# Kernel optimization log

Hardware: AMD Instinct MI355X
Metric: run time of the kernel (lower is better)

## Reference

```python
import math
import jax, jax.numpy as jnp
import numpy as np

B, L, D = 16, 2048, 64  # batch, seq len (m == n, self-attention), head dim
C = 30                   # ProbSparse sampling factor c


def setup_inputs() -> dict:
    key = jax.random.key(0)
    kq, kk, kv = jax.random.split(key, 3)
    Q = jax.random.normal(kq, (B, L, D), dtype=jnp.float32)
    K = jax.random.normal(kk, (B, L, D), dtype=jnp.float32)
    V = jax.random.normal(kv, (B, L, D), dtype=jnp.float32)
    return {"Q": Q, "K": K, "V": V, "seed": 0}


def reference(Q, K, V, seed):
    b, m, d = Q.shape
    n = K.shape[1]
    u = int(C * math.log(m))              # number of active queries
    U = min(int(m * math.log(n)), n)      # number of sampled keys (clamped to n)
    inv_sqrt_d = 1.0 / math.sqrt(d)

    rngs = jax.random.split(jax.random.key(seed), b)

    def _each_sample(Qb, Kb, Vb, r):
        # random sample of U key rows without replacement
        idx = jax.random.choice(r, n, shape=(U,), replace=False)
        Kbar = Kb[idx]                                # [U, d]
        Sbar = jnp.matmul(Qb, Kbar.T)                 # [m, U]
        M = jnp.max(Sbar, axis=1) - jnp.mean(Sbar, axis=1)  # sparsity measure [m]
        _, I = jax.lax.top_k(M, u)                    # active query indices [u]
        Qbar = Qb[I]                                  # [u, d]
        A = jax.nn.softmax(jnp.matmul(Qbar, Kb.T) * inv_sqrt_d, axis=-1)  # [u, n]
        S1 = jnp.matmul(A, Vb)                        # [u, d]
        # literal source: fill with mean(V, axis=1, keepdims=True) -> (n,1) broadcast (m==n)
        S = jnp.broadcast_to(jnp.mean(Vb, axis=1, keepdims=True), (m, d))
        return S.at[I].set(S1)

    return jax.vmap(_each_sample)(Q, K, V, rngs)
```

## Files before the change

kernel.cpp:

```cpp
#include <hip/hip_runtime.h>

#define NB 16
#define NN 2048
#define DH 64
#define NSEL 228
#define KS 8
#define CHUNK (NN / KS)
#define RS 4
#define EPSBAND 2.0e-3f

using s16x8 = __attribute__((ext_vector_type(8))) short;
using f32x16 = __attribute__((ext_vector_type(16))) float;

static __device__ __forceinline__ unsigned short f2bf(float x) {
  unsigned int u = __float_as_uint(x);
  u += 0x7fffu + ((u >> 16) & 1u);
  return (unsigned short)(u >> 16);
}
static __device__ __forceinline__ float bf2f(unsigned short h) {
  return __uint_as_float(((unsigned int)h) << 16);
}
static __device__ __forceinline__ unsigned int enc(float f) {
  unsigned int u = __float_as_uint(f);
  return (u & 0x80000000u) ? ~u : (u | 0x80000000u);
}
static __device__ __forceinline__ float dec(unsigned int k) {
  return (k & 0x80000000u) ? __uint_as_float(k & 0x7fffffffu)
                           : __uint_as_float(~k);
}

__global__ __launch_bounds__(256) void convk_kernel(const float* __restrict__ K,
                                                    unsigned short* __restrict__ Khi,
                                                    unsigned short* __restrict__ Klo) {
  const size_t e = ((size_t)blockIdx.x * 256 + threadIdx.x) * 8;
  float4 a = *(const float4*)(K + e);
  float4 b = *(const float4*)(K + e + 4);
  float v[8] = {a.x, a.y, a.z, a.w, b.x, b.y, b.z, b.w};
  union { unsigned short u[8]; s16x8 s; } H, L;
  #pragma unroll
  for (int j = 0; j < 8; ++j) {
    unsigned short h = f2bf(v[j]);
    H.u[j] = h;
    L.u[j] = f2bf(v[j] - bf2f(h));
  }
  *(s16x8*)(Khi + e) = H.s;
  *(s16x8*)(Klo + e) = L.s;
}

__global__ __launch_bounds__(256) void kcolsum_kernel(const float* __restrict__ K,
                                                      float* __restrict__ Kpart) {
  __shared__ float part[4][64];
  const int b = blockIdx.y, ch = blockIdx.x;
  const int d = threadIdx.x & 63, g = threadIdx.x >> 6;
  const float* Kb = K + ((size_t)b * NN + ch * 128) * DH;
  float s = 0.f;
  for (int r = g; r < 128; r += 4) s += Kb[r * DH + d];
  part[g][d] = s;
  __syncthreads();
  if (threadIdx.x < 64)
    Kpart[((size_t)b * 16 + ch) * 64 + threadIdx.x] =
        part[0][threadIdx.x] + part[1][threadIdx.x] +
        part[2][threadIdx.x] + part[3][threadIdx.x];
}

__global__ __launch_bounds__(256, 4) void rowstat_mfma(const float* __restrict__ Q,
                                                       const unsigned short* __restrict__ Khi,
                                                       const unsigned short* __restrict__ Klo,
                                                       float* __restrict__ Mmax) {
  __shared__ __align__(16) unsigned short KHs[128 * 64];
  __shared__ __align__(16) unsigned short KLs[128 * 64];
  const int b = blockIdx.y, cz = blockIdx.z;
  const int qbase = blockIdx.x * 128;
  const int tid = threadIdx.x;
  const int w = tid >> 6, lane = tid & 63;
  const int l31 = lane & 31, hi5 = lane >> 5;

  s16x8 qh[4], ql[4];
  {
    const float* qrow = Q + ((size_t)b * NN + qbase + w * 32 + l31) * DH;
    #pragma unroll
    for (int ks = 0; ks < 4; ++ks) {
      const int d0 = ks * 16 + hi5 * 8;
      float4 x = *(const float4*)(qrow + d0);
      float4 y = *(const float4*)(qrow + d0 + 4);
      float v[8] = {x.x, x.y, x.z, x.w, y.x, y.y, y.z, y.w};
      union { unsigned short u[8]; s16x8 s; } H, L;
      #pragma unroll
      for (int j = 0; j < 8; ++j) {
        unsigned short h = f2bf(v[j]);
        H.u[j] = h;
        L.u[j] = f2bf(v[j] - bf2f(h));
      }
      qh[ks] = H.s;
      ql[ks] = L.s;
    }
  }

  const size_t kbase = ((size_t)b * NN + cz * (NN / RS)) * DH;
  f32x16 vmax;
  #pragma unroll
  for (int i = 0; i < 16; ++i) vmax[i] = -3.0e38f;

  const int sr = tid >> 1;
  const int sh = tid & 1;

  for (int stage = 0; stage < NN / RS / 128; ++stage) {
    __syncthreads();
    {
      const size_t g = kbase + (size_t)(stage * 128 + sr) * DH + sh * 32;
      const unsigned short* gh = Khi + g;
      const unsigned short* gl = Klo + g;
      #pragma unroll
      for (int c = 0; c < 4; ++c) {
        s16x8 hv = *(const s16x8*)(gh + c * 8);
        s16x8 lv = *(const s16x8*)(gl + c * 8);
        const int chn = (sh * 4 + c) ^ (sr & 7);
        *(s16x8*)&KHs[(sr * 8 + chn) * 8] = hv;
        *(s16x8*)&KLs[(sr * 8 + chn) * 8] = lv;
      }
    }
    __syncthreads();

    #pragma unroll
    for (int ksub = 0; ksub < 4; ++ksub) {
      const int kr = ksub * 32 + l31;
      f32x16 acc;
      #pragma unroll
      for (int i = 0; i < 16; ++i) acc[i] = 0.f;
      #pragma unroll
      for (int ks = 0; ks < 4; ++ks) {
        const int chn = (ks * 2 + hi5) ^ (kr & 7);
        s16x8 ah = *(const s16x8*)&KHs[(kr * 8 + chn) * 8];
        s16x8 al = *(const s16x8*)&KLs[(kr * 8 + chn) * 8];
        acc = __builtin_amdgcn_mfma_f32_32x32x16_bf16(ah, qh[ks], acc, 0, 0, 0);
        acc = __builtin_amdgcn_mfma_f32_32x32x16_bf16(al, qh[ks], acc, 0, 0, 0);
        acc = __builtin_amdgcn_mfma_f32_32x32x16_bf16(ah, ql[ks], acc, 0, 0, 0);
      }
      #pragma unroll
      for (int i = 0; i < 16; ++i) vmax[i] = fmaxf(vmax[i], acc[i]);
    }
  }

  float m = vmax[0];
  #pragma unroll
  for (int i = 1; i < 16; ++i) m = fmaxf(m, vmax[i]);
  m = fmaxf(m, __shfl_xor(m, 32));
  if (lane < 32)
    Mmax[((size_t)cz * NB + b) * NN + qbase + w * 32 + lane] = m;
}

static __device__ unsigned int radix_thresh(const unsigned int* kreg, int lane,
                                            int wid, int* red) {
  unsigned int v = 0u;
  for (int bit = 31; bit >= 0; --bit) {
    const unsigned int cand = v | (1u << bit);
    int c = 0;
    #pragma unroll
    for (int f = 0; f < 8; ++f) c += (kreg[f] >= cand) ? 1 : 0;
    #pragma unroll
    for (int off = 1; off < 64; off <<= 1) c += __shfl_xor(c, off);
    if (lane == 0) red[wid] = c;
    __syncthreads();
    if (red[0] + red[1] + red[2] + red[3] >= NSEL) v = cand;
    __syncthreads();
  }
  return v;
}

__global__ __launch_bounds__(256) void select_kernel(const float* __restrict__ Q,
                                                     const float* __restrict__ K,
                                                     const float* __restrict__ Mmax,
                                                     const float* __restrict__ Kpart,
                                                     int* __restrict__ Isel) {
  __shared__ unsigned int keys[NN];
  __shared__ float meanv[NN];
  __shared__ int list_[NN];
  __shared__ float qsh[64];
  __shared__ float Ksl[64];
  __shared__ float fred[4];
  __shared__ int red[4];
  __shared__ int cntS;
  const int b = blockIdx.x;
  const int tid = threadIdx.x;
  const int lane = tid & 63, wid = tid >> 6;
  const int base = tid * 8;

  if (tid < 64) {
    float s = 0.f;
    for (int c = 0; c < 16; ++c) s += Kpart[((size_t)b * 16 + c) * 64 + tid];
    Ksl[tid] = s;
  }
  if (tid == 0) cntS = 0;
  __syncthreads();

  for (int f = 0; f < 8; ++f) {
    const int i = base + f;
    float mv = -3.0e38f;
    #pragma unroll
    for (int cz = 0; cz < RS; ++cz)
      mv = fmaxf(mv, Mmax[((size_t)cz * NB + b) * NN + i]);
    const float* qrow = Q + ((size_t)b * NN + i) * DH;
    float s = 0.f;
    #pragma unroll
    for (int d4 = 0; d4 < 16; ++d4) {
      float4 qv = *(const float4*)(qrow + d4 * 4);
      s = fmaf(qv.x, Ksl[d4 * 4 + 0], s);
      s = fmaf(qv.y, Ksl[d4 * 4 + 1], s);
      s = fmaf(qv.z, Ksl[d4 * 4 + 2], s);
      s = fmaf(qv.w, Ksl[d4 * 4 + 3], s);
    }
    const float mean = s * (1.0f / NN);
    meanv[i] = mean;
    keys[i] = enc(mv - mean);
  }
  __syncthreads();

  unsigned int kreg[8];
  #pragma unroll
  for (int f = 0; f < 8; ++f) kreg[f] = keys[base + f];

  const unsigned int v1 = radix_thresh(kreg, lane, wid, red);
  const float vf = dec(v1);

  #pragma unroll
  for (int f = 0; f < 8; ++f) {
    if (fabsf(dec(kreg[f]) - vf) <= EPSBAND) {
      int p = atomicAdd(&cntS, 1);
      list_[p] = base + f;
    }
  }
  __syncthreads();
  const int nband = cntS;
  for (int n = 0; n < nband; ++n) {
    const int row = list_[n];
    if (tid < 64) qsh[tid] = Q[((size_t)b * NN + row) * DH + tid];
    __syncthreads();
    float lmax = -3.0e38f;
    for (int j = tid; j < NN; j += 256) {
      const float* krow = K + ((size_t)b * NN + j) * DH;
      float s = 0.f;
      #pragma unroll
      for (int d4 = 0; d4 < 16; ++d4) {
        float4 kv = *(const float4*)(krow + d4 * 4);
        s = fmaf(kv.x, qsh[d4 * 4 + 0], s);
        s = fmaf(kv.y, qsh[d4 * 4 + 1], s);
        s = fmaf(kv.z, qsh[d4 * 4 + 2], s);
        s = fmaf(kv.w, qsh[d4 * 4 + 3], s);
      }
      lmax = fmaxf(lmax, s);
    }
    #pragma unroll
    for (int off = 1; off < 64; off <<= 1) lmax = fmaxf(lmax, __shfl_xor(lmax, off));
    if (lane == 0) fred[wid] = lmax;
    __syncthreads();
    if (tid == 0) {
      const float mx = fmaxf(fmaxf(fred[0], fred[1]), fmaxf(fred[2], fred[3]));
      keys[row] = enc(mx - meanv[row]);
    }
    __syncthreads();
  }
  #pragma unroll
  for (int f = 0; f < 8; ++f) kreg[f] = keys[base + f];

  const unsigned int v2 = radix_thresh(kreg, lane, wid, red);

  int flg[8];
  int cnt = 0;
  #pragma unroll
  for (int f = 0; f < 8; ++f) { flg[f] = (kreg[f] > v2) ? 1 : 0; cnt += flg[f]; }
  int scan = cnt;
  #pragma unroll
  for (int off = 1; off < 64; off <<= 1) {
    const int t = __shfl_up(scan, off);
    if (lane >= off) scan += t;
  }
  if (lane == 63) red[wid] = scan;
  __syncthreads();
  int wbase = 0;
  for (int ww = 0; ww < wid; ++ww) wbase += red[ww];
  const int cg = red[0] + red[1] + red[2] + red[3];
  int pos = wbase + scan - cnt;
  #pragma unroll
  for (int f = 0; f < 8; ++f)
    if (flg[f]) { Isel[b * NSEL + pos] = base + f; ++pos; }
  __syncthreads();

  const int need = NSEL - cg;
  cnt = 0;
  #pragma unroll
  for (int f = 0; f < 8; ++f) { flg[f] = (kreg[f] == v2) ? 1 : 0; cnt += flg[f]; }
  scan = cnt;
  #pragma unroll
  for (int off = 1; off < 64; off <<= 1) {
    const int t = __shfl_up(scan, off);
    if (lane >= off) scan += t;
  }
  if (lane == 63) red[wid] = scan;
  __syncthreads();
  wbase = 0;
  for (int ww = 0; ww < wid; ++ww) wbase += red[ww];
  pos = wbase + scan - cnt;
  #pragma unroll
  for (int f = 0; f < 8; ++f)
    if (flg[f]) {
      if (pos < need) Isel[b * NSEL + cg + pos] = base + f;
      ++pos;
    }
}

__global__ __launch_bounds__(256) void fill_kernel(const float* __restrict__ V,
                                                   float* __restrict__ out) {
  const size_t row = (size_t)blockIdx.x * 4 + (threadIdx.x >> 6);
  const int lane = threadIdx.x & 63;
  float x = V[row * DH + lane];
  #pragma unroll
  for (int off = 1; off < 64; off <<= 1) x += __shfl_xor(x, off);
  out[row * DH + lane] = x * (1.0f / DH);
}

__global__ __launch_bounds__(256) void attn_part_kernel(const float* __restrict__ Q,
                                                        const float* __restrict__ K,
                                                        const float* __restrict__ V,
                                                        const int* __restrict__ Isel,
                                                        float* __restrict__ Pm,
                                                        float* __restrict__ Pl,
                                                        float* __restrict__ Po) {
  __shared__ float Qt[64][32];
  __shared__ float Kt[64][64];
  __shared__ float Vs[64][64];
  __shared__ float Pt[64][36];
  const int b = blockIdx.z;
  const int kc = blockIdx.y;
  const int g = blockIdx.x;
  const int tid = threadIdx.x;
  const int wq = tid >> 5;
  const int kx = tid & 31;

  if (tid < 128) {
    const int rr = tid >> 2;
    const int dblk = (tid & 3) * 16;
    const int lq = g * 32 + rr;
    const int qidx = (lq < NSEL) ? Isel[b * NSEL + lq] : 0;
    const float* qs = Q + ((size_t)b * NN + qidx) * DH + dblk;
    #pragma unroll
    for (int f = 0; f < 4; ++f) {
      float4 v = *reinterpret_cast<const float4*>(qs + f * 4);
      Qt[dblk + f * 4 + 0][rr] = v.x;
      Qt[dblk + f * 4 + 1][rr] = v.y;
      Qt[dblk + f * 4 + 2][rr] = v.z;
      Qt[dblk + f * 4 + 3][rr] = v.w;
    }
  }

  const float* Kb = K + ((size_t)b * NN + kc * CHUNK) * DH;
  const float* Vb = V + ((size_t)b * NN + kc * CHUNK) * DH;

  float m[4], lp[4], o[4][2];
  #pragma unroll
  for (int a = 0; a < 4; ++a) {
    m[a] = -3.0e38f; lp[a] = 0.f; o[a][0] = 0.f; o[a][1] = 0.f;
  }

  for (int st = 0; st < CHUNK / 64; ++st) {
    __syncthreads();
    {
      const int rr = tid & 63;
      const int dblk = (tid >> 6) * 16;
      const float* ks = Kb + ((size_t)(st * 64 + rr)) * DH + dblk;
      #pragma unroll
      for (int f = 0; f < 4; ++f) {
        float4 v = *reinterpret_cast<const float4*>(ks + f * 4);
        Kt[dblk + f * 4 + 0][rr] = v.x;
        Kt[dblk + f * 4 + 1][rr] = v.y;
        Kt[dblk + f * 4 + 2][rr] = v.z;
        Kt[dblk + f * 4 + 3][rr] = v.w;
      }
      const float* vsrc = Vb + (size_t)st * 64 * DH;
      float* vdst = &Vs[0][0];
      #pragma unroll
      for (int it = 0; it < 4; ++it) {
        const int fo = (it * 256 + tid) * 4;
        *reinterpret_cast<float4*>(vdst + fo) =
            *reinterpret_cast<const float4*>(vsrc + fo);
      }
    }
    __syncthreads();

    float sc[4][2];
    #pragma unroll
    for (int a = 0; a < 4; ++a) { sc[a][0] = 0.f; sc[a][1] = 0.f; }
    #pragma unroll 4
    for (int d = 0; d < 64; ++d) {
      float qv[4];
      *reinterpret_cast<float4*>(qv) =
          *reinterpret_cast<const float4*>(&Qt[d][wq * 4]);
      const float2 kv = *reinterpret_cast<const float2*>(&Kt[d][kx * 2]);
      #pragma unroll
      for (int a = 0; a < 4; ++a) {
        sc[a][0] = fmaf(qv[a], kv.x, sc[a][0]);
        sc[a][1] = fmaf(qv[a], kv.y, sc[a][1]);
      }
    }
    #pragma unroll
    for (int a = 0; a < 4; ++a) { sc[a][0] *= 0.125f; sc[a][1] *= 0.125f; }

    float tm[4];
    #pragma unroll
    for (int a = 0; a < 4; ++a) tm[a] = fmaxf(sc[a][0], sc[a][1]);
    #pragma unroll
    for (int off = 1; off < 32; off <<= 1) {
      #pragma unroll
      for (int a = 0; a < 4; ++a) tm[a] = fmaxf(tm[a], __shfl_xor(tm[a], off));
    }

    float w0[4], w1[4];
    #pragma unroll
    for (int a = 0; a < 4; ++a) {
      const float mn = fmaxf(m[a], tm[a]);
      const float scale = __expf(m[a] - mn);
      m[a] = mn;
      lp[a] *= scale;
      o[a][0] *= scale;
      o[a][1] *= scale;
      w0[a] = __expf(sc[a][0] - mn);
      w1[a] = __expf(sc[a][1] - mn);
      lp[a] += w0[a] + w1[a];
    }
    *reinterpret_cast<float4*>(&Pt[kx * 2][wq * 4]) =
        make_float4(w0[0], w0[1], w0[2], w0[3]);
    *reinterpret_cast<float4*>(&Pt[kx * 2 + 1][wq * 4]) =
        make_float4(w1[0], w1[1], w1[2], w1[3]);
    __syncthreads();

    #pragma unroll 4
    for (int k = 0; k < 64; ++k) {
      float pv[4];
      *reinterpret_cast<float4*>(pv) =
          *reinterpret_cast<const float4*>(&Pt[k][wq * 4]);
      const float2 vv = *reinterpret_cast<const float2*>(&Vs[k][kx * 2]);
      #pragma unroll
      for (int a = 0; a < 4; ++a) {
        o[a][0] = fmaf(pv[a], vv.x, o[a][0]);
        o[a][1] = fmaf(pv[a], vv.y, o[a][1]);
      }
    }
  }

  #pragma unroll
  for (int off = 1; off < 32; off <<= 1) {
    #pragma unroll
    for (int a = 0; a < 4; ++a) lp[a] += __shfl_xor(lp[a], off);
  }

  #pragma unroll
  for (int a = 0; a < 4; ++a) {
    const int lq = g * 32 + wq * 4 + a;
    if (lq < NSEL) {
      const size_t row = ((size_t)b * NSEL + lq) * KS + kc;
      if (kx == 0) { Pm[row] = m[a]; Pl[row] = lp[a]; }
      *reinterpret_cast<float2*>(Po + row * 64 + kx * 2) =
          make_float2(o[a][0], o[a][1]);
    }
  }
}

__global__ __launch_bounds__(256) void combine_kernel(const int* __restrict__ Isel,
                                                      const float* __restrict__ Pm,
                                                      const float* __restrict__ Pl,
                                                      const float* __restrict__ Po,
                                                      float* __restrict__ out) {
  const int r = blockIdx.x * 4 + (threadIdx.x >> 6);
  if (r >= NB * NSEL) return;
  const int lane = threadIdx.x & 63;
  const int b = r / NSEL;
  const int qidx = Isel[r];
  const size_t base = (size_t)r * KS;

  float pm[KS];
  float gm = -3.0e38f;
  #pragma unroll
  for (int c = 0; c < KS; ++c) { pm[c] = Pm[base + c]; gm = fmaxf(gm, pm[c]); }
  float L = 0.f, od = 0.f;
  #pragma unroll
  for (int c = 0; c < KS; ++c) {
    const float e = __expf(pm[c] - gm);
    L += Pl[base + c] * e;
    od += Po[(base + c) * 64 + lane] * e;
  }
  out[((size_t)b * NN + qidx) * DH + lane] = od / L;
}

extern "C" void kernel_launch(void* const* d_in, const int* in_sizes, int n_in,
                              void* d_out, int out_size, void* d_ws, size_t ws_size,
                              hipStream_t stream) {
  const float* Q = (const float*)d_in[0];
  const float* K = (const float*)d_in[1];
  const float* V = (const float*)d_in[2];
  float* out = (float*)d_out;

  float* Mmax = (float*)d_ws;
  float* Kpart = Mmax + (size_t)RS * NB * NN;
  int* Isel = (int*)(Kpart + (size_t)NB * 16 * 64);
  float* Pm = (float*)(Isel + NB * NSEL);
  float* Pl = Pm + (size_t)NB * NSEL * KS;
  float* Po = Pl + (size_t)NB * NSEL * KS;
  unsigned short* Khi = (unsigned short*)(Po + (size_t)NB * NSEL * KS * 64);
  unsigned short* Klo = Khi + (size_t)NB * NN * DH;

  convk_kernel<<<dim3((NB * NN * DH) / (256 * 8)), 256, 0, stream>>>(K, Khi, Klo);
  kcolsum_kernel<<<dim3(16, NB), 256, 0, stream>>>(K, Kpart);
  rowstat_mfma<<<dim3(NN / 128, NB, RS), 256, 0, stream>>>(Q, Khi, Klo, Mmax);
  select_kernel<<<dim3(NB), 256, 0, stream>>>(Q, K, Mmax, Kpart, Isel);
  fill_kernel<<<dim3(NB * NN / 4), 256, 0, stream>>>(V, out);
  attn_part_kernel<<<dim3(8, KS, NB), 256, 0, stream>>>(Q, K, V, Isel, Pm, Pl, Po);
  combine_kernel<<<dim3((NB * NSEL + 3) / 4), 256, 0, stream>>>(Isel, Pm, Pl, Po, out);
}
```

Measured before the change: 242.0 us.

## Split serial select kernel into parallel mstat, radix, recheck, radix stages

The single-block-per-batch select kernel becomes four kernels. A wide mstat kernel computes the sparsity keys and means. A radix pass finds the band of borderline rows. A recheck kernel spreads exact max recomputation for band rows over up to 32 blocks per batch. A second radix pass picks the final indices. This targets the per-batch serial work, especially the sequential band-row loop, which ran on only 16 blocks; the cost is extra launches and round trips to global memory for keys and means.

```diff
diff --git a/kernel.cpp b/kernel.cpp
--- a/kernel.cpp
+++ b/kernel.cpp
@@ -8,6 +8,7 @@
 #define CHUNK (NN / KS)
 #define RS 4
 #define EPSBAND 2.0e-3f
+#define MAXB 32
 
 using s16x8 = __attribute__((ext_vector_type(8))) short;
 using f32x16 = __attribute__((ext_vector_type(16))) float;
@@ -149,6 +150,42 @@
     Mmax[((size_t)cz * NB + b) * NN + qbase + w * 32 + lane] = m;
 }
 
+__global__ __launch_bounds__(256) void mstat_kernel(const float* __restrict__ Q,
+                                                    const float* __restrict__ Mmax,
+                                                    const float* __restrict__ Kpart,
+                                                    unsigned int* __restrict__ keysW,
+                                                    float* __restrict__ meanv) {
+  __shared__ float Ksl[64];
+  const int b = blockIdx.y;
+  const int seg = blockIdx.x;
+  const int tid = threadIdx.x;
+  if (tid < 64) {
+    float s = 0.f;
+    #pragma unroll
+    for (int c = 0; c < 16; ++c) s += Kpart[((size_t)b * 16 + c) * 64 + tid];
+    Ksl[tid] = s;
+  }
+  __syncthreads();
+  const int i = seg * 256 + tid;
+  float mv = -3.0e38f;
+  #pragma unroll
+  for (int cz = 0; cz < RS; ++cz)
+    mv = fmaxf(mv, Mmax[((size_t)cz * NB + b) * NN + i]);
+  const float* qrow = Q + ((size_t)b * NN + i) * DH;
+  float s = 0.f;
+  #pragma unroll
+  for (int d4 = 0; d4 < 16; ++d4) {
+    float4 qv = *(const float4*)(qrow + d4 * 4);
+    s = fmaf(qv.x, Ksl[d4 * 4 + 0], s);
+    s = fmaf(qv.y, Ksl[d4 * 4 + 1], s);
+    s = fmaf(qv.z, Ksl[d4 * 4 + 2], s);
+    s = fmaf(qv.w, Ksl[d4 * 4 + 3], s);
+  }
+  const float mean = s * (1.0f / NN);
+  meanv[(size_t)b * NN + i] = mean;
+  keysW[(size_t)b * NN + i] = enc(mv - mean);
+}
+
 static __device__ unsigned int radix_thresh(const unsigned int* kreg, int lane,
                                             int wid, int* red) {
   unsigned int v = 0u;
@@ -167,17 +204,9 @@
   return v;
 }
 
-__global__ __launch_bounds__(256) void select_kernel(const float* __restrict__ Q,
-                                                     const float* __restrict__ K,
-                                                     const float* __restrict__ Mmax,
-                                                     const float* __restrict__ Kpart,
-                                                     int* __restrict__ Isel) {
-  __shared__ unsigned int keys[NN];
-  __shared__ float meanv[NN];
-  __shared__ int list_[NN];
-  __shared__ float qsh[64];
-  __shared__ float Ksl[64];
-  __shared__ float fred[4];
+__global__ __launch_bounds__(256) void radix1_kernel(const unsigned int* __restrict__ keysW,
+                                                     int* __restrict__ Band,
+                                                     int* __restrict__ nband) {
   __shared__ int red[4];
   __shared__ int cntS;
   const int b = blockIdx.x;
@@ -185,39 +214,11 @@
   const int lane = tid & 63, wid = tid >> 6;
   const int base = tid * 8;
 
-  if (tid < 64) {
-    float s = 0.f;
-    for (int c = 0; c < 16; ++c) s += Kpart[((size_t)b * 16 + c) * 64 + tid];
-    Ksl[tid] = s;
-  }
+  unsigned int kreg[8];
+  #pragma unroll
+  for (int f = 0; f < 8; ++f) kreg[f] = keysW[(size_t)b * NN + base + f];
   if (tid == 0) cntS = 0;
   __syncthreads();
-
-  for (int f = 0; f < 8; ++f) {
-    const int i = base + f;
-    float mv = -3.0e38f;
-    #pragma unroll
-    for (int cz = 0; cz < RS; ++cz)
-      mv = fmaxf(mv, Mmax[((size_t)cz * NB + b) * NN + i]);
-    const float* qrow = Q + ((size_t)b * NN + i) * DH;
-    float s = 0.f;
-    #pragma unroll
-    for (int d4 = 0; d4 < 16; ++d4) {
-      float4 qv = *(const float4*)(qrow + d4 * 4);
-      s = fmaf(qv.x, Ksl[d4 * 4 + 0], s);
-      s = fmaf(qv.y, Ksl[d4 * 4 + 1], s);
-      s = fmaf(qv.z, Ksl[d4 * 4 + 2], s);
-      s = fmaf(qv.w, Ksl[d4 * 4 + 3], s);
-    }
-    const float mean = s * (1.0f / NN);
-    meanv[i] = mean;
-    keys[i] = enc(mv - mean);
-  }
-  __syncthreads();
-
-  unsigned int kreg[8];
-  #pragma unroll
-  for (int f = 0; f < 8; ++f) kreg[f] = keys[base + f];
 
   const unsigned int v1 = radix_thresh(kreg, lane, wid, red);
   const float vf = dec(v1);
@@ -226,13 +227,29 @@
   for (int f = 0; f < 8; ++f) {
     if (fabsf(dec(kreg[f]) - vf) <= EPSBAND) {
       int p = atomicAdd(&cntS, 1);
-      list_[p] = base + f;
-    }
-  }
-  __syncthreads();
-  const int nband = cntS;
-  for (int n = 0; n < nband; ++n) {
-    const int row = list_[n];
+      Band[(size_t)b * NN + p] = base + f;
+    }
+  }
+  __syncthreads();
+  if (tid == 0) nband[b] = cntS;
+}
+
+__global__ __launch_bounds__(256) void recheck_kernel(const float* __restrict__ Q,
+                                                      const float* __restrict__ K,
+                                                      const int* __restrict__ Band,
+                                                      const int* __restrict__ nband,
+                                                      const float* __restrict__ meanv,
+                                                      unsigned int* __restrict__ keysW) {
+  __shared__ float qsh[64];
+  __shared__ float fred[4];
+  const int b = blockIdx.y;
+  const int nb_ = nband[b];
+  const int tid = threadIdx.x;
+  const int lane = tid & 63, wid = tid >> 6;
+
+  for (int n = blockIdx.x; n < nb_; n += MAXB) {
+    const int row = Band[(size_t)b * NN + n];
+    __syncthreads();
     if (tid < 64) qsh[tid] = Q[((size_t)b * NN + row) * DH + tid];
     __syncthreads();
     float lmax = -3.0e38f;
@@ -250,17 +267,29 @@
       lmax = fmaxf(lmax, s);
     }
     #pragma unroll
-    for (int off = 1; off < 64; off <<= 1) lmax = fmaxf(lmax, __shfl_xor(lmax, off));
+    for (int off = 1; off < 64; off <<= 1)
+      lmax = fmaxf(lmax, __shfl_xor(lmax, off));
     if (lane == 0) fred[wid] = lmax;
     __syncthreads();
     if (tid == 0) {
       const float mx = fmaxf(fmaxf(fred[0], fred[1]), fmaxf(fred[2], fred[3]));
-      keys[row] = enc(mx - meanv[row]);
-    }
-    __syncthreads();
-  }
-  #pragma unroll
-  for (int f = 0; f < 8; ++f) kreg[f] = keys[base + f];
+      keysW[(size_t)b * NN + row] = enc(mx - meanv[(size_t)b * NN + row]);
+    }
+  }
+}
+
+__global__ __launch_bounds__(256) void radix2_kernel(const unsigned int* __restrict__ keysW,
+                                                     int* __restrict__ Isel) {
+  __shared__ int red[4];
+  const int b = blockIdx.x;
+  const int tid = threadIdx.x;
+  const int lane = tid & 63, wid = tid >> 6;
+  const int base = tid * 8;
+
+  unsigned int kreg[8];
+  #pragma unroll
+  for (int f = 0; f < 8; ++f) kreg[f] = keysW[(size_t)b * NN + base + f];
+  __syncthreads();
 
   const unsigned int v2 = radix_thresh(kreg, lane, wid, red);
 
@@ -500,7 +529,11 @@
 
   float* Mmax = (float*)d_ws;
   float* Kpart = Mmax + (size_t)RS * NB * NN;
-  int* Isel = (int*)(Kpart + (size_t)NB * 16 * 64);
+  unsigned int* keysW = (unsigned int*)(Kpart + (size_t)NB * 16 * 64);
+  float* meanv = (float*)(keysW + (size_t)NB * NN);
+  int* Band = (int*)(meanv + (size_t)NB * NN);
+  int* nband = Band + (size_t)NB * NN;
+  int* Isel = nband + 16;
   float* Pm = (float*)(Isel + NB * NSEL);
   float* Pl = Pm + (size_t)NB * NSEL * KS;
   float* Po = Pl + (size_t)NB * NSEL * KS;
@@ -510,7 +543,10 @@
   convk_kernel<<<dim3((NB * NN * DH) / (256 * 8)), 256, 0, stream>>>(K, Khi, Klo);
   kcolsum_kernel<<<dim3(16, NB), 256, 0, stream>>>(K, Kpart);
   rowstat_mfma<<<dim3(NN / 128, NB, RS), 256, 0, stream>>>(Q, Khi, Klo, Mmax);
-  select_kernel<<<dim3(NB), 256, 0, stream>>>(Q, K, Mmax, Kpart, Isel);
+  mstat_kernel<<<dim3(8, NB), 256, 0, stream>>>(Q, Mmax, Kpart, keysW, meanv);
+  radix1_kernel<<<dim3(NB), 256, 0, stream>>>(keysW, Band, nband);
+  recheck_kernel<<<dim3(MAXB, NB), 256, 0, stream>>>(Q, K, Band, nband, meanv, keysW);
+  radix2_kernel<<<dim3(NB), 256, 0, stream>>>(keysW, Isel);
   fill_kernel<<<dim3(NB * NN / 4), 256, 0, stream>>>(V, out);
   attn_part_kernel<<<dim3(8, KS, NB), 256, 0, stream>>>(Q, K, V, Isel, Pm, Pl, Po);
   combine_kernel<<<dim3((NB * NSEL + 3) / 4), 256, 0, stream>>>(Isel, Pm, Pl, Po, out);
```

Measured after the change: 248.5 us. 1.03x slower.
